# Performance work log

Hardware: AMD Instinct MI355X
Metric: run time of the kernel (lower is better)

Reference implementation:

```python
import jax, jax.numpy as jnp
import numpy as np

RATIO = 1.0  # self.ratio from __init__


def setup_inputs() -> dict:
    key = jax.random.key(0)
    ks = jax.random.split(key, 12)
    B, C, N = 128, 2048, 196
    S, L, M = 312, 300, 1024  # attritube_num, w2v_length, med_dim
    inp = {
        "feat": jax.random.normal(ks[0], (B, C, N), dtype=jnp.float32),
        "att_emb": jax.random.normal(ks[1], (S, L), dtype=jnp.float32),
        # Linear params (PyTorch layout: W is [out, in], y = x @ W.T + b)
        "Wq": jax.random.normal(ks[2], (M, L), dtype=jnp.float32) * (1.0 / np.sqrt(L)),
        "bq": jnp.zeros((M,), dtype=jnp.float32),
        "Wk": jax.random.normal(ks[3], (M, C), dtype=jnp.float32) * (1.0 / np.sqrt(C)),
        "bk": jnp.zeros((M,), dtype=jnp.float32),
        "Wv": jax.random.normal(ks[4], (M, C), dtype=jnp.float32) * (1.0 / np.sqrt(C)),
        "bv": jnp.zeros((M,), dtype=jnp.float32),
        "Wo": jax.random.normal(ks[5], (C, M), dtype=jnp.float32) * (1.0 / np.sqrt(M)),
        "bo": jnp.zeros((C,), dtype=jnp.float32),
        "V_final": jax.random.normal(ks[6], (S, C), dtype=jnp.float32),
    }
    return inp


def reference(feat, att_emb, Wq, bq, Wk, bk, Wv, bv, Wo, bo, V_final):
    # feat: [B, C, N], att_emb: [S, L]
    query = att_emb @ Wq.T + bq                      # [S, M]
    feat_t = jnp.swapaxes(feat, 1, 2)                # [B, N, C]
    k = feat_t @ Wk.T + bk                           # [B, N, M]
    v = feat_t @ Wv.T + bv                           # [B, N, M]
    scores = jnp.einsum('sm,bnm->bsn', query, k)     # [B, S, N]
    attn = jax.nn.softmax(scores, axis=-1)           # softmax over N (dim=2)
    attented = jnp.einsum('bsn,bnm->bsm', attn, v)   # [B, S, M]
    attented_o = attented @ Wo.T + bo                # [B, S, C]
    feat_pool = jnp.mean(feat, axis=-1)              # avg_pool1d(kernel=N) -> [B, C]
    final = feat_pool[:, None, :] + RATIO * attented_o  # [B, S, C]
    v2s = jnp.einsum('bsc,sc->bs', final, V_final)   # [B, S]
    return v2s
```

## Files before the change

kernel.cpp:

```cpp
#include <hip/hip_runtime.h>
#include <hip/hip_bf16.h>
#include <cstdint>

typedef _Float16 half_t;
typedef _Float16 f16x8 __attribute__((ext_vector_type(8), aligned(16)));
typedef _Float16 f16x4 __attribute__((ext_vector_type(4), aligned(8)));
typedef _Float16 f16x2 __attribute__((ext_vector_type(2), aligned(4)));
typedef float f32x4 __attribute__((ext_vector_type(4)));

#define B_ 128
#define C_ 2048
#define N_ 196
#define S_ 312
#define L_ 300
#define LP 320
#define M_ 1024
#define NP 224
#define SP 384

__device__ __forceinline__ void gload16(const half_t* g, half_t* l) {
    __builtin_amdgcn_global_load_lds((const __attribute__((address_space(1))) void*)g,
                                     (__attribute__((address_space(3))) void*)l, 16, 0, 0);
}

__global__ __launch_bounds__(256) void k_convert(const float* __restrict__ att, const float* __restrict__ Wq,
                                                 const float* __restrict__ V, const float* __restrict__ Wo,
                                                 const float* __restrict__ bv, half_t* __restrict__ atth,
                                                 half_t* __restrict__ wqh, half_t* __restrict__ vh,
                                                 float* __restrict__ Wobv) {
    int z = blockIdx.z;
    if (z == 3) {
        if (blockIdx.x >= 512) return;
        int c = blockIdx.x * 4 + (threadIdx.x >> 6);
        int lane = threadIdx.x & 63;
        const float* wr_ = Wo + (size_t)c * M_;
        float acc = 0;
#pragma unroll
        for (int i = 0; i < 16; ++i) acc += wr_[lane + 64 * i] * bv[lane + 64 * i];
        for (int off = 32; off; off >>= 1) acc += __shfl_xor(acc, off);
        if (lane == 0) Wobv[c] = acc;
        return;
    }
    size_t e = ((size_t)blockIdx.x * 256 + threadIdx.x) * 4;
    if (z == 0) {
        if (e >= (size_t)SP * LP) return;
        int r = (int)(e / LP), c = (int)(e % LP);
        f16x4 h;
#pragma unroll
        for (int j = 0; j < 4; ++j) h[j] = (half_t)((r < S_ && c + j < L_) ? att[(size_t)r * L_ + c + j] : 0.f);
        *(f16x4*)&atth[e] = h;
    } else if (z == 1) {
        if (e >= (size_t)M_ * LP) return;
        int r = (int)(e / LP), c = (int)(e % LP);
        f16x4 h;
#pragma unroll
        for (int j = 0; j < 4; ++j) h[j] = (half_t)((c + j < L_) ? Wq[(size_t)r * L_ + c + j] : 0.f);
        *(f16x4*)&wqh[e] = h;
    } else {
        if (e >= (size_t)SP * C_) return;
        int r = (int)(e / C_);
        f16x4 h;
        if (r < S_) {
            float4 v = *(const float4*)&V[e];
            h[0] = (half_t)v.x; h[1] = (half_t)v.y; h[2] = (half_t)v.z; h[3] = (half_t)v.w;
        } else {
            h[0] = h[1] = h[2] = h[3] = (half_t)0.f;
        }
        *(f16x4*)&vh[e] = h;
    }
}

__global__ __launch_bounds__(256) void k_transp3(const float* __restrict__ Wk, const float* __restrict__ Wo,
                                                 const float* __restrict__ Wv, half_t* __restrict__ WkT,
                                                 half_t* __restrict__ WoT, half_t* __restrict__ WvT) {
    __shared__ __attribute__((aligned(16))) half_t lsT[64][72];
    int z = blockIdx.z;
    const float* in; half_t* out; int R, Cc;
    if (z == 0)      { in = Wk; out = WkT; R = 1024; Cc = 2048; }
    else if (z == 1) { in = Wo; out = WoT; R = 2048; Cc = 1024; }
    else             { in = Wv; out = WvT; R = 1024; Cc = 2048; }
    if ((int)blockIdx.x >= Cc / 64 || (int)blockIdx.y >= R / 64) return;
    int c0 = blockIdx.x * 64, r0 = blockIdx.y * 64;
    int t = threadIdx.x;
#pragma unroll
    for (int i = 0; i < 4; ++i) {
        int Q = t + 256 * i;
        int rq = Q >> 5, cq = Q & 31;
        int rr = 2 * rq, cc = 2 * cq;
        const float* p0 = in + (size_t)(r0 + rr) * Cc + c0 + cc;
        float2 va = *(const float2*)p0;
        float2 vb = *(const float2*)(p0 + Cc);
        f16x2 w0; w0[0] = (half_t)va.x; w0[1] = (half_t)vb.x;
        f16x2 w1; w1[0] = (half_t)va.y; w1[1] = (half_t)vb.y;
        *(f16x2*)&lsT[cc][rr]     = w0;
        *(f16x2*)&lsT[cc + 1][rr] = w1;
    }
    __syncthreads();
    int cl = t >> 2, ch = t & 3;
    f16x8 v0 = *(const f16x8*)&lsT[cl][ch * 16];
    f16x8 v1 = *(const f16x8*)&lsT[cl][ch * 16 + 8];
    half_t* po = out + (size_t)(c0 + cl) * R + r0 + ch * 16;
    *(f16x8*)po = v0;
    *(f16x8*)(po + 8) = v1;
}

struct GDesc {
    const half_t* A; const half_t* Bm;
    float* outF; half_t* outH; const float* bias;
    int kdim; int ldo; int rowmul; int rowoff;
};

__global__ __launch_bounds__(256) void k_prep(GDesc d0, GDesc d1) {
    GDesc d = blockIdx.z ? d1 : d0;
    __shared__ __attribute__((aligned(16))) half_t lsA[3][128 * 32];
    __shared__ __attribute__((aligned(16))) half_t lsB[3][128 * 32];
    int t = threadIdx.x;
    int wid = t >> 6, lane = t & 63;
    const int rA0 = blockIdx.y * 128, rB0 = blockIdx.x * 128;
    int wr = wid >> 1, wc = wid & 1;
    int g = lane >> 4, l15 = lane & 15;
    const int r_ = t >> 2;
    const int gsrc = ((t & 3) ^ ((t >> 3) & 3)) * 8;
    const int kdim = d.kdim;
    const half_t* pA  = d.A + (size_t)(rA0 + r_) * kdim + gsrc;
    const half_t* pA2 = pA + (size_t)64 * kdim;
    const half_t* pB  = d.Bm + (size_t)(rB0 + r_) * kdim + gsrc;
    const half_t* pB2 = pB + (size_t)64 * kdim;
    const int lo = t * 8;
    const int xsw = ((l15 >> 1) & 3) * 8;
    f32x4 acc[4][4] = {};
    int nk = kdim >> 5;

#define STAGE(slot, kc)                              \
    do {                                             \
        gload16(pA + (kc), &lsA[slot][lo]);          \
        gload16(pA2 + (kc), &lsA[slot][lo + 2048]);  \
        gload16(pB + (kc), &lsB[slot][lo]);          \
        gload16(pB2 + (kc), &lsB[slot][lo + 2048]);  \
    } while (0)

    STAGE(0, 0);
    STAGE(1, 32);
    int cur = 0, nxt = 2;
    for (int tk = 0; tk < nk; ++tk) {
        if (tk == nk - 1) asm volatile("s_waitcnt vmcnt(0)" ::: "memory");
        else              asm volatile("s_waitcnt vmcnt(4)" ::: "memory");
        __builtin_amdgcn_s_barrier();
        __builtin_amdgcn_sched_barrier(0);
        f16x8 af[4], bf[4];
#pragma unroll
        for (int i = 0; i < 4; ++i) af[i] = *(const f16x8*)&lsA[cur][(wr * 64 + i * 16 + l15) * 32 + ((g * 8) ^ xsw)];
#pragma unroll
        for (int j = 0; j < 4; ++j) bf[j] = *(const f16x8*)&lsB[cur][(wc * 64 + j * 16 + l15) * 32 + ((g * 8) ^ xsw)];
        if (tk + 2 < nk) STAGE(nxt, (tk + 2) * 32);
#pragma unroll
        for (int i = 0; i < 4; ++i)
#pragma unroll
            for (int j = 0; j < 4; ++j)
                acc[i][j] = __builtin_amdgcn_mfma_f32_16x16x32_f16(af[i], bf[j], acc[i][j], 0, 0, 0);
        cur = (cur == 2) ? 0 : cur + 1;
        nxt = (nxt == 2) ? 0 : nxt + 1;
    }
#undef STAGE

#pragma unroll
    for (int i = 0; i < 4; ++i) {
        int r0 = rA0 + wr * 64 + i * 16 + g * 4;
#pragma unroll
        for (int j = 0; j < 4; ++j) {
            int c0 = rB0 + wc * 64 + j * 16 + l15;
            float bval = d.bias ? d.bias[c0] : 0.f;
#pragma unroll
            for (int qq = 0; qq < 4; ++qq) {
                int rr = (r0 + qq) * d.rowmul + d.rowoff;
                float val = acc[i][j][qq];
                if (d.outF) d.outF[(size_t)rr * d.ldo + c0] = val;
                if (d.outH) d.outH[(size_t)rr * d.ldo + c0] = (half_t)(val + bval);
            }
        }
    }
}

__global__ __launch_bounds__(256) void k_fused(const half_t* __restrict__ AstackP, const half_t* __restrict__ featT,
                                               const float* __restrict__ base2, float* __restrict__ out, int b0) {
    __shared__ __attribute__((aligned(16))) half_t lsA[2][192 * 32];
    __shared__ __attribute__((aligned(16))) half_t lsB[3][256 * 32];
    __shared__ float lsE[2][80][4];
    int t = threadIdx.x;
    int bb = blockIdx.x, st = blockIdx.y;
    int wid = t >> 6, lane = t & 63;
    int wr = wid >> 1, wc = wid & 1;
    int g = lane >> 4, l15 = lane & 15;
    const int gsrc = ((t & 3) ^ ((t >> 3) & 3)) * 8;
    const half_t* pA  = AstackP + ((size_t)st * 160 + (t >> 2)) * C_ + gsrc;
    const half_t* pA2 = pA + (size_t)64 * C_;
    const half_t* pA3 = pA + (size_t)128 * C_;
    const half_t* pB  = featT + ((size_t)bb * NP + (t >> 2)) * C_ + gsrc;
    const half_t* pB2 = pB + (size_t)64 * C_;
    const half_t* pB3 = pB + (size_t)128 * C_;
    const half_t* pB4 = pB + (size_t)192 * C_;
    const int lo = t * 8;
    const int xsw = ((l15 >> 1) & 3) * 8;
    f32x4 acc[5][7] = {};

#define FSTAGEA(slot, kc)                            \
    do {                                             \
        gload16(pA + (kc), &lsA[slot][lo]);          \
        gload16(pA2 + (kc), &lsA[slot][lo + 2048]);  \
        gload16(pA3 + (kc), &lsA[slot][lo + 4096]);  \
    } while (0)
#define FSTAGEB(slot, kc)                            \
    do {                                             \
        gload16(pB + (kc), &lsB[slot][lo]);          \
        gload16(pB2 + (kc), &lsB[slot][lo + 2048]);  \
        gload16(pB3 + (kc), &lsB[slot][lo + 4096]);  \
        gload16(pB4 + (kc), &lsB[slot][lo + 6144]);  \
    } while (0)

    FSTAGEA(0, 0);
    FSTAGEB(0, 0);
    FSTAGEB(1, 32);
    for (int tk = 0; tk < 64; ++tk) {
        int ca = tk & 1;
        int cb = tk % 3;
        if (tk == 63) asm volatile("s_waitcnt vmcnt(0)" ::: "memory");
        else          asm volatile("s_waitcnt vmcnt(4)" ::: "memory");
        __builtin_amdgcn_s_barrier();
        __builtin_amdgcn_sched_barrier(0);
        if (tk + 1 < 64) FSTAGEA(ca ^ 1, (tk + 1) * 32);
        if (tk + 2 < 64) FSTAGEB((tk + 2) % 3, (tk + 2) * 32);
        f16x8 af[5], bf[7];
#pragma unroll
        for (int i = 0; i < 5; ++i) af[i] = *(const f16x8*)&lsA[ca][(wr * 80 + i * 16 + l15) * 32 + ((g * 8) ^ xsw)];
#pragma unroll
        for (int j = 0; j < 7; ++j) bf[j] = *(const f16x8*)&lsB[cb][(wc * 112 + j * 16 + l15) * 32 + ((g * 8) ^ xsw)];
        asm volatile("s_waitcnt lgkmcnt(0)" ::: "memory");
        __builtin_amdgcn_sched_barrier(0);
#pragma unroll
        for (int i = 0; i < 5; ++i)
#pragma unroll
            for (int j = 0; j < 7; ++j)
                acc[i][j] = __builtin_amdgcn_mfma_f32_16x16x32_f16(af[i], bf[j], acc[i][j], 0, 0, 0);
    }
#undef FSTAGEA
#undef FSTAGEB

#pragma unroll
    for (int i = 0; i < 5; ++i) {
#pragma unroll
        for (int pair = 0; pair < 2; ++pair) {
            float m = -3.0e38f;
#pragma unroll
            for (int j = 0; j < 7; ++j) {
                int col = wc * 112 + j * 16 + l15;
                if (col < N_) m = fmaxf(m, acc[i][j][2 * pair]);
            }
#pragma unroll
            for (int off = 1; off < 16; off <<= 1) m = fmaxf(m, __shfl_xor(m, off));
            float ls = 0.f, dt = 0.f;
#pragma unroll
            for (int j = 0; j < 7; ++j) {
                int col = wc * 112 + j * 16 + l15;
                if (col < N_) {
                    float p = __expf(acc[i][j][2 * pair] - m);
                    ls += p;
                    dt += p * acc[i][j][2 * pair + 1];
                }
            }
#pragma unroll
            for (int off = 1; off < 16; off <<= 1) { ls += __shfl_xor(ls, off); dt += __shfl_xor(dt, off); }
            if (l15 == 0) {
                int pr = wr * 40 + i * 8 + g * 2 + pair;
                lsE[wc][pr][0] = m; lsE[wc][pr][1] = ls; lsE[wc][pr][2] = dt;
            }
        }
    }
    __syncthreads();
    if (t < 80) {
        float m0 = lsE[0][t][0], l0 = lsE[0][t][1], dv0 = lsE[0][t][2];
        float m1 = lsE[1][t][0], l1 = lsE[1][t][1], dv1 = lsE[1][t][2];
        float M = fmaxf(m0, m1);
        float e0 = __expf(m0 - M), e1 = __expf(m1 - M);
        float L = l0 * e0 + l1 * e1, D = dv0 * e0 + dv1 * e1;
        int s = st * 80 + t;
        if (s < S_) {
            int bg = b0 + bb;
            out[(size_t)bg * S_ + s] = base2[(size_t)bg * S_ + s] + D / L;
        }
    }
}

__global__ __launch_bounds__(256) void k_transf(const float* __restrict__ feat, half_t* __restrict__ featT,
                                                float* __restrict__ poolp) {
    __shared__ __attribute__((aligned(16))) half_t lsT[64][72];
    __shared__ float poolLs[64];
    int nT = blockIdx.x, cT = blockIdx.y, bb = blockIdx.z;
    int n0 = nT * 64, c0 = cT * 64;
    const float* fb = feat + (size_t)bb * C_ * N_;
    int t = threadIdx.x;
#pragma unroll
    for (int i = 0; i < 4; ++i) {
        int Q = t + 256 * i;
        int cq = Q >> 5, nq = Q & 31;
        int cc = 2 * cq, nn = 2 * nq;
        int n = n0 + nn;
        float2 va = {0, 0}, vb = {0, 0};
        if (n < N_) {
            const float* p0 = fb + (size_t)(c0 + cc) * N_ + n;
            va = *(const float2*)p0;
            vb = *(const float2*)(p0 + N_);
        }
        f16x2 w0; w0[0] = (half_t)va.x; w0[1] = (half_t)vb.x;
        f16x2 w1; w1[0] = (half_t)va.y; w1[1] = (half_t)vb.y;
        *(f16x2*)&lsT[nn][cc]     = w0;
        *(f16x2*)&lsT[nn + 1][cc] = w1;
        float sA = va.x + va.y, sB = vb.x + vb.y;
        for (int off = 16; off; off >>= 1) { sA += __shfl_xor(sA, off); sB += __shfl_xor(sB, off); }
        if ((t & 31) == 0) { poolLs[cc] = sA; poolLs[cc + 1] = sB; }
    }
    __syncthreads();
    int nl = t >> 2, ch = t & 3;
    int n = n0 + nl;
    if (n < NP) {
        f16x8 v0 = *(const f16x8*)&lsT[nl][ch * 16];
        f16x8 v1 = *(const f16x8*)&lsT[nl][ch * 16 + 8];
        half_t* po = featT + ((size_t)bb * NP + n) * C_ + c0 + ch * 16;
        *(f16x8*)po = v0;
        *(f16x8*)(po + 8) = v1;
    }
    if (t < 64) poolp[((size_t)nT * B_ + bb) * C_ + c0 + t] = poolLs[t];
}

__global__ __launch_bounds__(256) void k_poolv(const float* __restrict__ poolp, const float* __restrict__ bo,
                                               const float* __restrict__ Wobv, const float* __restrict__ V,
                                               float* __restrict__ base2) {
    int sc = blockIdx.x, b = blockIdx.y;
    __shared__ float w[C_];
    int t = threadIdx.x;
    for (int i = t; i < C_; i += 256) {
        float s = poolp[(size_t)b * C_ + i] + poolp[((size_t)B_ + b) * C_ + i] +
                  poolp[((size_t)2 * B_ + b) * C_ + i] + poolp[((size_t)3 * B_ + b) * C_ + i];
        w[i] = s * (1.0f / 196.0f) + bo[i] + Wobv[i];
    }
    __syncthreads();
    int wid = t >> 6, lane = t & 63;
    for (int s = sc * 78 + wid; s < sc * 78 + 78; s += 4) {
        const float* vr = V + (size_t)s * C_;
        float acc = 0;
#pragma unroll
        for (int i = 0; i < 32; ++i) acc += w[lane + 64 * i] * vr[lane + 64 * i];
        for (int off = 32; off; off >>= 1) acc += __shfl_xor(acc, off);
        if (lane == 0) base2[(size_t)b * S_ + s] = acc;
    }
}

extern "C" void kernel_launch(void* const* d_in, const int* in_sizes, int n_in,
                              void* d_out, int out_size, void* d_ws, size_t ws_size,
                              hipStream_t stream) {
    const float* feat = (const float*)d_in[0];
    const float* att  = (const float*)d_in[1];
    const float* Wq   = (const float*)d_in[2];
    const float* bq   = (const float*)d_in[3];
    const float* Wk   = (const float*)d_in[4];
    const float* Wv   = (const float*)d_in[6];
    const float* bv   = (const float*)d_in[7];
    const float* Wo   = (const float*)d_in[8];
    const float* bo   = (const float*)d_in[9];
    const float* V    = (const float*)d_in[10];
    float* out = (float*)d_out;

    auto AL = [](size_t x) { return (x + 255) & ~(size_t)255; };
    const size_t szAstk = (size_t)768 * C_ * 2;
    const size_t szQh   = (size_t)SP * M_ * 2;
    const size_t szVh   = (size_t)SP * C_ * 2;
    const size_t szUh   = (size_t)SP * M_ * 2;
    const size_t szWT   = (size_t)C_ * M_ * 2;
    const size_t szAtth = (size_t)SP * LP * 2;
    const size_t szWqh  = (size_t)M_ * LP * 2;
    const size_t szPoolp = (size_t)4 * B_ * C_ * 4;
    const size_t szBase = (size_t)B_ * S_ * 4;
    const size_t szWobv = (size_t)C_ * 4;
    size_t fixed = AL(szAstk) + AL(szQh) + AL(szVh) + AL(szUh) + 3 * AL(szWT) +
                   AL(szAtth) + AL(szWqh) + AL(szPoolp) + AL(szBase) + AL(szWobv);

    int nsplit = 1;
    while (nsplit < 32) {
        size_t nB = B_ / nsplit;
        size_t need = fixed + AL(nB * NP * C_ * 2 + 131072);
        if (need <= ws_size) break;
        nsplit *= 2;
    }
    int nB = B_ / nsplit;

    char* p = (char*)d_ws;
    half_t* AstackP = (half_t*)p; p += AL(szAstk);
    half_t* qh     = (half_t*)p; p += AL(szQh);
    half_t* Vh     = (half_t*)p; p += AL(szVh);
    half_t* Uh     = (half_t*)p; p += AL(szUh);
    half_t* WkT    = (half_t*)p; p += AL(szWT);
    half_t* WoT    = (half_t*)p; p += AL(szWT);
    half_t* WvT    = (half_t*)p; p += AL(szWT);
    half_t* atth   = (half_t*)p; p += AL(szAtth);
    half_t* wqh    = (half_t*)p; p += AL(szWqh);
    float*  poolp  = (float*)p;  p += AL(szPoolp);
    float*  base2  = (float*)p;  p += AL(szBase);
    float*  Wobv   = (float*)p;  p += AL(szWobv);
    half_t* featT  = (half_t*)p;

    k_convert<<<dim3(768, 1, 4), 256, 0, stream>>>(att, Wq, V, Wo, bv, atth, wqh, Vh, Wobv);
    k_transp3<<<dim3(32, 32, 3), 256, 0, stream>>>(Wk, Wo, Wv, WkT, WoT, WvT);
    {
        GDesc dq{atth, wqh, nullptr, qh, bq, LP, M_, 1, 0};
        GDesc dU{Vh, WoT, nullptr, Uh, nullptr, C_, M_, 1, 0};
        k_prep<<<dim3(8, 3, 2), 256, 0, stream>>>(dq, dU);
    }
    {
        GDesc dk{qh, WkT, nullptr, AstackP, nullptr, M_, C_, 2, 0};
        GDesc dv{Uh, WvT, nullptr, AstackP, nullptr, M_, C_, 2, 1};
        k_prep<<<dim3(16, 3, 2), 256, 0, stream>>>(dk, dv);
    }

    for (int h = 0; h < nsplit; ++h) {
        const float* fh = feat + (size_t)h * nB * C_ * N_;
        k_transf<<<dim3(4, 32, nB), 256, 0, stream>>>(fh, featT, poolp);
        k_poolv<<<dim3(4, nB), 256, 0, stream>>>(poolp, bo, Wobv, V, base2 + (size_t)h * nB * S_);
        k_fused<<<dim3(nB, 4), 256, 0, stream>>>(AstackP, featT, base2, out, h * nB);
    }
}
```

Before: 252.7 us.

## Merge independent prep kernels into combined launches to cut launch count

Weight conversion, weight transposes and the feature transpose/pool are merged into one flattened-grid kernel. The small Q/U GEMMs and the pooled-V projection are merged into a second kernel, so there are four launches instead of seven when nsplit is 1. The aim is to remove launch gaps and tail idle time between small dependent kernels by running independent work together. In exchange, the merged kernels take on the largest shared-memory footprint of their parts (48 KB in the second one), which may reduce occupancy for the lighter branches.

```diff
diff --git a/kernel.cpp b/kernel.cpp
--- a/kernel.cpp
+++ b/kernel.cpp
@@ -23,41 +23,34 @@
                                      (__attribute__((address_space(3))) void*)l, 16, 0, 0);
 }
 
-__global__ __launch_bounds__(256) void k_convert(const float* __restrict__ att, const float* __restrict__ Wq,
-                                                 const float* __restrict__ V, const float* __restrict__ Wo,
-                                                 const float* __restrict__ bv, half_t* __restrict__ atth,
-                                                 half_t* __restrict__ wqh, half_t* __restrict__ vh,
-                                                 float* __restrict__ Wobv) {
-    int z = blockIdx.z;
-    if (z == 3) {
-        if (blockIdx.x >= 512) return;
-        int c = blockIdx.x * 4 + (threadIdx.x >> 6);
-        int lane = threadIdx.x & 63;
-        const float* wr_ = Wo + (size_t)c * M_;
-        float acc = 0;
-#pragma unroll
-        for (int i = 0; i < 16; ++i) acc += wr_[lane + 64 * i] * bv[lane + 64 * i];
-        for (int off = 32; off; off >>= 1) acc += __shfl_xor(acc, off);
-        if (lane == 0) Wobv[c] = acc;
-        return;
-    }
-    size_t e = ((size_t)blockIdx.x * 256 + threadIdx.x) * 4;
-    if (z == 0) {
-        if (e >= (size_t)SP * LP) return;
-        int r = (int)(e / LP), c = (int)(e % LP);
+struct GDesc {
+    const half_t* A; const half_t* Bm;
+    float* outF; half_t* outH; const float* bias;
+    int kdim; int ldo; int rowmul; int rowoff;
+};
+
+
+__device__ __forceinline__ void dev_convert(int c, int t, const float* __restrict__ att,
+                                            const float* __restrict__ Wq, const float* __restrict__ V,
+                                            const float* __restrict__ Wo, const float* __restrict__ bv,
+                                            half_t* __restrict__ atth, half_t* __restrict__ wqh,
+                                            half_t* __restrict__ vh, float* __restrict__ Wobv) {
+    if (c < 120) {
+        size_t e = ((size_t)c * 256 + t) * 4;
+        int r = (int)(e / LP), cc = (int)(e % LP);
         f16x4 h;
 #pragma unroll
-        for (int j = 0; j < 4; ++j) h[j] = (half_t)((r < S_ && c + j < L_) ? att[(size_t)r * L_ + c + j] : 0.f);
+        for (int j = 0; j < 4; ++j) h[j] = (half_t)((r < S_ && cc + j < L_) ? att[(size_t)r * L_ + cc + j] : 0.f);
         *(f16x4*)&atth[e] = h;
-    } else if (z == 1) {
-        if (e >= (size_t)M_ * LP) return;
-        int r = (int)(e / LP), c = (int)(e % LP);
+    } else if (c < 440) {
+        size_t e = ((size_t)(c - 120) * 256 + t) * 4;
+        int r = (int)(e / LP), cc = (int)(e % LP);
         f16x4 h;
 #pragma unroll
-        for (int j = 0; j < 4; ++j) h[j] = (half_t)((c + j < L_) ? Wq[(size_t)r * L_ + c + j] : 0.f);
+        for (int j = 0; j < 4; ++j) h[j] = (half_t)((cc + j < L_) ? Wq[(size_t)r * L_ + cc + j] : 0.f);
         *(f16x4*)&wqh[e] = h;
-    } else {
-        if (e >= (size_t)SP * C_) return;
+    } else if (c < 1208) {
+        size_t e = ((size_t)(c - 440) * 256 + t) * 4;
         int r = (int)(e / C_);
         f16x4 h;
         if (r < S_) {
@@ -67,21 +60,29 @@
             h[0] = h[1] = h[2] = h[3] = (half_t)0.f;
         }
         *(f16x4*)&vh[e] = h;
-    }
-}
-
-__global__ __launch_bounds__(256) void k_transp3(const float* __restrict__ Wk, const float* __restrict__ Wo,
-                                                 const float* __restrict__ Wv, half_t* __restrict__ WkT,
-                                                 half_t* __restrict__ WoT, half_t* __restrict__ WvT) {
-    __shared__ __attribute__((aligned(16))) half_t lsT[64][72];
-    int z = blockIdx.z;
-    const float* in; half_t* out; int R, Cc;
-    if (z == 0)      { in = Wk; out = WkT; R = 1024; Cc = 2048; }
-    else if (z == 1) { in = Wo; out = WoT; R = 2048; Cc = 1024; }
-    else             { in = Wv; out = WvT; R = 1024; Cc = 2048; }
-    if ((int)blockIdx.x >= Cc / 64 || (int)blockIdx.y >= R / 64) return;
-    int c0 = blockIdx.x * 64, r0 = blockIdx.y * 64;
-    int t = threadIdx.x;
+    } else {
+        int cc = (c - 1208) * 4 + (t >> 6);
+        int lane = t & 63;
+        const float* wr_ = Wo + (size_t)cc * M_;
+        float acc = 0;
+#pragma unroll
+        for (int i = 0; i < 16; ++i) acc += wr_[lane + 64 * i] * bv[lane + 64 * i];
+        for (int off = 32; off; off >>= 1) acc += __shfl_xor(acc, off);
+        if (lane == 0) Wobv[cc] = acc;
+    }
+}
+
+__device__ __forceinline__ void dev_transp3(int r3, int t, const float* __restrict__ Wk,
+                                            const float* __restrict__ Wo, const float* __restrict__ Wv,
+                                            half_t* __restrict__ WkT, half_t* __restrict__ WoT,
+                                            half_t* __restrict__ WvT, char* smc) {
+    half_t (*lsT)[72] = (half_t(*)[72])smc;
+    int z = r3 >> 9, r = r3 & 511;
+    const float* in; half_t* out; int R, Cc, bx, by;
+    if (z == 0)      { in = Wk; out = WkT; R = 1024; Cc = 2048; bx = r & 31; by = r >> 5; }
+    else if (z == 1) { in = Wo; out = WoT; R = 2048; Cc = 1024; bx = r & 15; by = r >> 4; }
+    else             { in = Wv; out = WvT; R = 1024; Cc = 2048; bx = r & 31; by = r >> 5; }
+    int c0 = bx * 64, r0 = by * 64;
 #pragma unroll
     for (int i = 0; i < 4; ++i) {
         int Q = t + 256 * i;
@@ -104,19 +105,50 @@
     *(f16x8*)(po + 8) = v1;
 }
 
-struct GDesc {
-    const half_t* A; const half_t* Bm;
-    float* outF; half_t* outH; const float* bias;
-    int kdim; int ldo; int rowmul; int rowoff;
-};
-
-__global__ __launch_bounds__(256) void k_prep(GDesc d0, GDesc d1) {
-    GDesc d = blockIdx.z ? d1 : d0;
-    __shared__ __attribute__((aligned(16))) half_t lsA[3][128 * 32];
-    __shared__ __attribute__((aligned(16))) half_t lsB[3][128 * 32];
-    int t = threadIdx.x;
+__device__ __forceinline__ void dev_transf(const float* __restrict__ feat, half_t* __restrict__ featT,
+                                           float* __restrict__ poolp, int nT, int cT, int bb, int t, char* smc) {
+    half_t (*lsT)[72] = (half_t(*)[72])smc;
+    float* poolLs = (float*)(smc + 64 * 72 * 2);
+    int n0 = nT * 64, c0 = cT * 64;
+    const float* fb = feat + (size_t)bb * C_ * N_;
+#pragma unroll
+    for (int i = 0; i < 4; ++i) {
+        int Q = t + 256 * i;
+        int cq = Q >> 5, nq = Q & 31;
+        int cc = 2 * cq, nn = 2 * nq;
+        int n = n0 + nn;
+        float2 va = {0, 0}, vb = {0, 0};
+        if (n < N_) {
+            const float* p0 = fb + (size_t)(c0 + cc) * N_ + n;
+            va = *(const float2*)p0;
+            vb = *(const float2*)(p0 + N_);
+        }
+        f16x2 w0; w0[0] = (half_t)va.x; w0[1] = (half_t)vb.x;
+        f16x2 w1; w1[0] = (half_t)va.y; w1[1] = (half_t)vb.y;
+        *(f16x2*)&lsT[nn][cc]     = w0;
+        *(f16x2*)&lsT[nn + 1][cc] = w1;
+        float sA = va.x + va.y, sB = vb.x + vb.y;
+        for (int off = 16; off; off >>= 1) { sA += __shfl_xor(sA, off); sB += __shfl_xor(sB, off); }
+        if ((t & 31) == 0) { poolLs[cc] = sA; poolLs[cc + 1] = sB; }
+    }
+    __syncthreads();
+    int nl = t >> 2, ch = t & 3;
+    int n = n0 + nl;
+    if (n < NP) {
+        f16x8 v0 = *(const f16x8*)&lsT[nl][ch * 16];
+        f16x8 v1 = *(const f16x8*)&lsT[nl][ch * 16 + 8];
+        half_t* po = featT + ((size_t)bb * NP + n) * C_ + c0 + ch * 16;
+        *(f16x8*)po = v0;
+        *(f16x8*)(po + 8) = v1;
+    }
+    if (t < 64) poolp[((size_t)nT * B_ + bb) * C_ + c0 + t] = poolLs[t];
+}
+
+__device__ __forceinline__ void dev_prep(GDesc d, int bx, int by, int t, char* smc) {
+    half_t* lsA = (half_t*)smc;
+    half_t* lsB = lsA + 3 * 4096;
     int wid = t >> 6, lane = t & 63;
-    const int rA0 = blockIdx.y * 128, rB0 = blockIdx.x * 128;
+    const int rA0 = by * 128, rB0 = bx * 128;
     int wr = wid >> 1, wc = wid & 1;
     int g = lane >> 4, l15 = lane & 15;
     const int r_ = t >> 2;
@@ -131,16 +163,16 @@
     f32x4 acc[4][4] = {};
     int nk = kdim >> 5;
 
-#define STAGE(slot, kc)                              \
-    do {                                             \
-        gload16(pA + (kc), &lsA[slot][lo]);          \
-        gload16(pA2 + (kc), &lsA[slot][lo + 2048]);  \
-        gload16(pB + (kc), &lsB[slot][lo]);          \
-        gload16(pB2 + (kc), &lsB[slot][lo + 2048]);  \
+#define PSTAGE(slot, kc)                                    \
+    do {                                                    \
+        gload16(pA + (kc), &lsA[(slot) * 4096 + lo]);       \
+        gload16(pA2 + (kc), &lsA[(slot) * 4096 + lo + 2048]); \
+        gload16(pB + (kc), &lsB[(slot) * 4096 + lo]);       \
+        gload16(pB2 + (kc), &lsB[(slot) * 4096 + lo + 2048]); \
     } while (0)
 
-    STAGE(0, 0);
-    STAGE(1, 32);
+    PSTAGE(0, 0);
+    PSTAGE(1, 32);
     int cur = 0, nxt = 2;
     for (int tk = 0; tk < nk; ++tk) {
         if (tk == nk - 1) asm volatile("s_waitcnt vmcnt(0)" ::: "memory");
@@ -149,10 +181,10 @@
         __builtin_amdgcn_sched_barrier(0);
         f16x8 af[4], bf[4];
 #pragma unroll
-        for (int i = 0; i < 4; ++i) af[i] = *(const f16x8*)&lsA[cur][(wr * 64 + i * 16 + l15) * 32 + ((g * 8) ^ xsw)];
-#pragma unroll
-        for (int j = 0; j < 4; ++j) bf[j] = *(const f16x8*)&lsB[cur][(wc * 64 + j * 16 + l15) * 32 + ((g * 8) ^ xsw)];
-        if (tk + 2 < nk) STAGE(nxt, (tk + 2) * 32);
+        for (int i = 0; i < 4; ++i) af[i] = *(const f16x8*)&lsA[cur * 4096 + (wr * 64 + i * 16 + l15) * 32 + ((g * 8) ^ xsw)];
+#pragma unroll
+        for (int j = 0; j < 4; ++j) bf[j] = *(const f16x8*)&lsB[cur * 4096 + (wc * 64 + j * 16 + l15) * 32 + ((g * 8) ^ xsw)];
+        if (tk + 2 < nk) PSTAGE(nxt, (tk + 2) * 32);
 #pragma unroll
         for (int i = 0; i < 4; ++i)
 #pragma unroll
@@ -161,7 +193,7 @@
         cur = (cur == 2) ? 0 : cur + 1;
         nxt = (nxt == 2) ? 0 : nxt + 1;
     }
-#undef STAGE
+#undef PSTAGE
 
 #pragma unroll
     for (int i = 0; i < 4; ++i) {
@@ -179,6 +211,85 @@
             }
         }
     }
+}
+
+__device__ __forceinline__ void dev_poolv(const float* __restrict__ poolp, const float* __restrict__ bo,
+                                          const float* __restrict__ Wobv, const float* __restrict__ V,
+                                          float* __restrict__ base2, int sc, int b, int t, char* smc) {
+    float* w = (float*)smc;
+    for (int i = t; i < C_; i += 256) {
+        float s = poolp[(size_t)b * C_ + i] + poolp[((size_t)B_ + b) * C_ + i] +
+                  poolp[((size_t)2 * B_ + b) * C_ + i] + poolp[((size_t)3 * B_ + b) * C_ + i];
+        w[i] = s * (1.0f / 196.0f) + bo[i] + Wobv[i];
+    }
+    __syncthreads();
+    int wid = t >> 6, lane = t & 63;
+    for (int s = sc * 78 + wid; s < sc * 78 + 78; s += 4) {
+        const float* vr = V + (size_t)s * C_;
+        float acc = 0;
+#pragma unroll
+        for (int i = 0; i < 32; ++i) acc += w[lane + 64 * i] * vr[lane + 64 * i];
+        for (int off = 32; off; off >>= 1) acc += __shfl_xor(acc, off);
+        if (lane == 0) base2[(size_t)b * S_ + s] = acc;
+    }
+}
+
+
+__global__ __launch_bounds__(256) void k_d1(const float* __restrict__ feat, const float* __restrict__ att,
+                                            const float* __restrict__ Wq, const float* __restrict__ V,
+                                            const float* __restrict__ Wo, const float* __restrict__ bv,
+                                            const float* __restrict__ Wk, const float* __restrict__ Wv,
+                                            half_t* __restrict__ featT, float* __restrict__ poolp,
+                                            half_t* __restrict__ atth, half_t* __restrict__ wqh,
+                                            half_t* __restrict__ vh, float* __restrict__ Wobv,
+                                            half_t* __restrict__ WkT, half_t* __restrict__ WoT,
+                                            half_t* __restrict__ WvT) {
+    __shared__ __attribute__((aligned(16))) char sm[9472];
+    int x = blockIdx.x, t = threadIdx.x;
+    if (x < 16384) {
+        dev_transf(feat, featT, poolp, x & 3, (x >> 2) & 31, x >> 7, t, sm);
+    } else if (x < 16384 + 1720) {
+        dev_convert(x - 16384, t, att, Wq, V, Wo, bv, atth, wqh, vh, Wobv);
+    } else {
+        dev_transp3(x - 16384 - 1720, t, Wk, Wo, Wv, WkT, WoT, WvT, sm);
+    }
+}
+
+__global__ __launch_bounds__(256) void k_d2(GDesc dq, GDesc dU, const float* __restrict__ poolp,
+                                            const float* __restrict__ bo, const float* __restrict__ Wobv,
+                                            const float* __restrict__ V, float* __restrict__ base2) {
+    __shared__ __attribute__((aligned(16))) char sm[49152];
+    int x = blockIdx.x, t = threadIdx.x;
+    if (x < 48) {
+        dev_prep((x / 24) ? dU : dq, x & 7, (x >> 3) % 3, t, sm);
+    } else {
+        int r = x - 48;
+        dev_poolv(poolp, bo, Wobv, V, base2, r & 3, r >> 2, t, sm);
+    }
+}
+
+__global__ __launch_bounds__(256) void k_prep2(GDesc d0, GDesc d1) {
+    __shared__ __attribute__((aligned(16))) char sm[49152];
+    dev_prep(blockIdx.z ? d1 : d0, blockIdx.x, blockIdx.y, threadIdx.x, sm);
+}
+
+__global__ __launch_bounds__(256) void k_misc(const float* att, const float* Wq, const float* V,
+                                              const float* Wo, const float* bv, const float* Wk,
+                                              const float* Wv, half_t* atth, half_t* wqh, half_t* vh,
+                                              float* Wobv, half_t* WkT, half_t* WoT, half_t* WvT) {
+    __shared__ __attribute__((aligned(16))) char sm[9472];
+    int x = blockIdx.x, t = threadIdx.x;
+    if (x < 1720) dev_convert(x, t, att, Wq, V, Wo, bv, atth, wqh, vh, Wobv);
+    else          dev_transp3(x - 1720, t, Wk, Wo, Wv, WkT, WoT, WvT, sm);
+}
+__global__ __launch_bounds__(256) void k_transf_only(const float* feat, half_t* featT, float* poolp) {
+    __shared__ __attribute__((aligned(16))) char sm[9472];
+    dev_transf(feat, featT, poolp, blockIdx.x, blockIdx.y, blockIdx.z, threadIdx.x, sm);
+}
+__global__ __launch_bounds__(256) void k_poolv_only(const float* poolp, const float* bo, const float* Wobv,
+                                                    const float* V, float* base2) {
+    __shared__ __attribute__((aligned(16))) char sm[8192];
+    dev_poolv(poolp, bo, Wobv, V, base2, blockIdx.x, blockIdx.y, threadIdx.x, sm);
 }
 
 __global__ __launch_bounds__(256) void k_fused(const half_t* __restrict__ AstackP, const half_t* __restrict__ featT,
@@ -290,70 +401,6 @@
     }
 }
 
-__global__ __launch_bounds__(256) void k_transf(const float* __restrict__ feat, half_t* __restrict__ featT,
-                                                float* __restrict__ poolp) {
-    __shared__ __attribute__((aligned(16))) half_t lsT[64][72];
-    __shared__ float poolLs[64];
-    int nT = blockIdx.x, cT = blockIdx.y, bb = blockIdx.z;
-    int n0 = nT * 64, c0 = cT * 64;
-    const float* fb = feat + (size_t)bb * C_ * N_;
-    int t = threadIdx.x;
-#pragma unroll
-    for (int i = 0; i < 4; ++i) {
-        int Q = t + 256 * i;
-        int cq = Q >> 5, nq = Q & 31;
-        int cc = 2 * cq, nn = 2 * nq;
-        int n = n0 + nn;
-        float2 va = {0, 0}, vb = {0, 0};
-        if (n < N_) {
-            const float* p0 = fb + (size_t)(c0 + cc) * N_ + n;
-            va = *(const float2*)p0;
-            vb = *(const float2*)(p0 + N_);
-        }
-        f16x2 w0; w0[0] = (half_t)va.x; w0[1] = (half_t)vb.x;
-        f16x2 w1; w1[0] = (half_t)va.y; w1[1] = (half_t)vb.y;
-        *(f16x2*)&lsT[nn][cc]     = w0;
-        *(f16x2*)&lsT[nn + 1][cc] = w1;
-        float sA = va.x + va.y, sB = vb.x + vb.y;
-        for (int off = 16; off; off >>= 1) { sA += __shfl_xor(sA, off); sB += __shfl_xor(sB, off); }
-        if ((t & 31) == 0) { poolLs[cc] = sA; poolLs[cc + 1] = sB; }
-    }
-    __syncthreads();
-    int nl = t >> 2, ch = t & 3;
-    int n = n0 + nl;
-    if (n < NP) {
-        f16x8 v0 = *(const f16x8*)&lsT[nl][ch * 16];
-        f16x8 v1 = *(const f16x8*)&lsT[nl][ch * 16 + 8];
-        half_t* po = featT + ((size_t)bb * NP + n) * C_ + c0 + ch * 16;
-        *(f16x8*)po = v0;
-        *(f16x8*)(po + 8) = v1;
-    }
-    if (t < 64) poolp[((size_t)nT * B_ + bb) * C_ + c0 + t] = poolLs[t];
-}
-
-__global__ __launch_bounds__(256) void k_poolv(const float* __restrict__ poolp, const float* __restrict__ bo,
-                                               const float* __restrict__ Wobv, const float* __restrict__ V,
-                                               float* __restrict__ base2) {
-    int sc = blockIdx.x, b = blockIdx.y;
-    __shared__ float w[C_];
-    int t = threadIdx.x;
-    for (int i = t; i < C_; i += 256) {
-        float s = poolp[(size_t)b * C_ + i] + poolp[((size_t)B_ + b) * C_ + i] +
-                  poolp[((size_t)2 * B_ + b) * C_ + i] + poolp[((size_t)3 * B_ + b) * C_ + i];
-        w[i] = s * (1.0f / 196.0f) + bo[i] + Wobv[i];
-    }
-    __syncthreads();
-    int wid = t >> 6, lane = t & 63;
-    for (int s = sc * 78 + wid; s < sc * 78 + 78; s += 4) {
-        const float* vr = V + (size_t)s * C_;
-        float acc = 0;
-#pragma unroll
-        for (int i = 0; i < 32; ++i) acc += w[lane + 64 * i] * vr[lane + 64 * i];
-        for (int off = 32; off; off >>= 1) acc += __shfl_xor(acc, off);
-        if (lane == 0) base2[(size_t)b * S_ + s] = acc;
-    }
-}
-
 extern "C" void kernel_launch(void* const* d_in, const int* in_sizes, int n_in,
                               void* d_out, int out_size, void* d_ws, size_t ws_size,
                               hipStream_t stream) {
@@ -407,23 +454,28 @@
     float*  Wobv   = (float*)p;  p += AL(szWobv);
     half_t* featT  = (half_t*)p;
 
-    k_convert<<<dim3(768, 1, 4), 256, 0, stream>>>(att, Wq, V, Wo, bv, atth, wqh, Vh, Wobv);
-    k_transp3<<<dim3(32, 32, 3), 256, 0, stream>>>(Wk, Wo, Wv, WkT, WoT, WvT);
-    {
-        GDesc dq{atth, wqh, nullptr, qh, bq, LP, M_, 1, 0};
-        GDesc dU{Vh, WoT, nullptr, Uh, nullptr, C_, M_, 1, 0};
-        k_prep<<<dim3(8, 3, 2), 256, 0, stream>>>(dq, dU);
-    }
-    {
-        GDesc dk{qh, WkT, nullptr, AstackP, nullptr, M_, C_, 2, 0};
-        GDesc dv{Uh, WvT, nullptr, AstackP, nullptr, M_, C_, 2, 1};
-        k_prep<<<dim3(16, 3, 2), 256, 0, stream>>>(dk, dv);
-    }
-
-    for (int h = 0; h < nsplit; ++h) {
-        const float* fh = feat + (size_t)h * nB * C_ * N_;
-        k_transf<<<dim3(4, 32, nB), 256, 0, stream>>>(fh, featT, poolp);
-        k_poolv<<<dim3(4, nB), 256, 0, stream>>>(poolp, bo, Wobv, V, base2 + (size_t)h * nB * S_);
-        k_fused<<<dim3(nB, 4), 256, 0, stream>>>(AstackP, featT, base2, out, h * nB);
-    }
-}
+    GDesc dq{atth, wqh, nullptr, qh, bq, LP, M_, 1, 0};
+    GDesc dU{Vh, WoT, nullptr, Uh, nullptr, C_, M_, 1, 0};
+    GDesc dk{qh, WkT, nullptr, AstackP, nullptr, M_, C_, 2, 0};
+    GDesc dv{Uh, WvT, nullptr, AstackP, nullptr, M_, C_, 2, 1};
+
+    if (nsplit == 1) {
+        k_d1<<<dim3(16384 + 1720 + 1536), 256, 0, stream>>>(feat, att, Wq, V, Wo, bv, Wk, Wv,
+                                                            featT, poolp, atth, wqh, Vh, Wobv,
+                                                            WkT, WoT, WvT);
+        k_d2<<<dim3(560), 256, 0, stream>>>(dq, dU, poolp, bo, Wobv, V, base2);
+        k_prep2<<<dim3(16, 3, 2), 256, 0, stream>>>(dk, dv);
+        k_fused<<<dim3(B_, 4), 256, 0, stream>>>(AstackP, featT, base2, out, 0);
+    } else {
+        k_misc<<<dim3(1720 + 1536), 256, 0, stream>>>(att, Wq, V, Wo, bv, Wk, Wv,
+                                                      atth, wqh, Vh, Wobv, WkT, WoT, WvT);
+        k_prep2<<<dim3(8, 3, 2), 256, 0, stream>>>(dq, dU);
+        k_prep2<<<dim3(16, 3, 2), 256, 0, stream>>>(dk, dv);
+        for (int h = 0; h < nsplit; ++h) {
+            const float* fh = feat + (size_t)h * nB * C_ * N_;
+            k_transf_only<<<dim3(4, 32, nB), 256, 0, stream>>>(fh, featT, poolp);
+            k_poolv_only<<<dim3(4, nB), 256, 0, stream>>>(poolp, bo, Wobv, V, base2 + (size_t)h * nB * S_);
+            k_fused<<<dim3(nB, 4), 256, 0, stream>>>(AstackP, featT, base2, out, h * nB);
+        }
+    }
+}
```

After: 218.1 us. -13.7%, faster.
